# Kernel optimization log

Measured on AMD Instinct MI355X. Metric: run time of the kernel, lower is better.

Reference implementation:

```python
import jax, jax.numpy as jnp
import numpy as np

V, FN, CIN, HID, PTS = 50000, 100000, 3, 256, 10000
TEMP = 0.1
EPS = 1e-20


def line_mesh_graph(f, Vn):
    # f: [F,3] int triangles. Build the 'line mesh': one node per unique mesh edge.
    fe = jnp.concatenate([f[:, :2], f[:, 1:], f[:, jnp.array([2, 0])]], 0)  # [3F,2]
    fe = jnp.sort(fe, axis=1)
    keys = fe[:, 0] * Vn + fe[:, 1]                       # [3F] unique key per undirected edge
    ukeys, inv = jnp.unique(keys, return_inverse=True)
    edge_node = jnp.stack([ukeys // Vn, ukeys % Vn], -1)  # [E,2] endpoints of each edge-node
    E = ukeys.shape[0]
    feid = inv.reshape(3, -1).T                           # [F,3] edge-node id per face edge
    # line-graph connectivity: edges of the same face are mutual neighbors, plus self-loops
    srcs, dsts = [], []
    for i, j in ((0, 1), (1, 0), (1, 2), (2, 1), (2, 0), (0, 2)):
        srcs.append(feid[:, i]); dsts.append(feid[:, j])
    loop = jnp.arange(E)
    edge = jnp.stack([jnp.concatenate(srcs + [loop]), jnp.concatenate(dsts + [loop])], 0)  # [2,NE]
    return edge, edge_node, keys


def gsn_conv(x, edge, Ws, Wn, b):
    # GSNConv stand-in: self transform + mean-aggregated neighbor transform
    s, d = edge[0], edge[1]
    N = x.shape[0]
    deg = jax.ops.segment_sum(jnp.ones_like(s, x.dtype), d, num_segments=N)
    agg = jax.ops.segment_sum(x[s], d, num_segments=N) / jnp.clip(deg, 1.0)[:, None]
    return x @ Ws + agg @ Wn + b


def gumbel_mask(logits, temperature, num, key):
    U = jax.random.uniform(key, logits.shape)
    g = -jnp.log(-jnp.log(U + EPS) + EPS)
    y = jax.nn.softmax((logits + g) / temperature, -1)[:, 0]  # [E]
    _, ind = jax.lax.top_k(y, num)
    y_hard = jnp.zeros_like(y).at[ind].set(1.0)
    mask = jax.lax.stop_gradient(y_hard - y) + y              # straight-through one-hot
    return mask, y_hard == 1.0


def mesh_collapse(f, keys, pool_edge, Vn):
    # Vectorized replacement of the per-pool-edge python loop: hash-join pooled edge keys
    # against all 3F face-edge keys via sorted search.
    PE = pool_edge.shape[0]
    pool_idx = jnp.arange(Vn, Vn + PE)
    edge_keys = keys.reshape(3, -1).T                     # [F,3] (cols: e01,e12,e20)
    pk = pool_edge[:, 0] * Vn + pool_edge[:, 1]
    order = jnp.argsort(pk); pks = pk[order]
    flat = edge_keys.reshape(-1)
    pos = jnp.clip(jnp.searchsorted(pks, flat), 0, PE - 1)
    found = pks[pos] == flat
    pei = jnp.where(found, pool_idx[order[pos]], -1).reshape(-1, 3)  # pool_edge_idx [F,3]
    fm = found.reshape(-1, 3)
    pen = fm.sum(1)                                       # pool_edge_num per face
    psi = (fm * jnp.arange(3)).sum(1)                     # pool_start_idx per face
    vv = jnp.stack([f[:, 0], pei[:, 0], f[:, 1], pei[:, 1], f[:, 2], pei[:, 2]], -1)
    nf0 = f[pen == 0]
    fv1 = vv[pen == 1]; s1 = psi[pen == 1]
    fv1 = jnp.concatenate([fv1[s1 == 0], jnp.roll(fv1[s1 == 1], -2, 1), jnp.roll(fv1[s1 == 2], 2, 1)], 0)
    nf1 = jnp.concatenate([jnp.stack([fv1[:, 0], fv1[:, 1], fv1[:, 4]], -1),
                           jnp.stack([fv1[:, 1], fv1[:, 2], fv1[:, 4]], -1)], 0)
    fv2 = vv[pen == 2]; s2 = psi[pen == 2]
    fv2 = jnp.concatenate([fv2[s2 == 1], jnp.roll(fv2[s2 == 2], 2, 1), jnp.roll(fv2[s2 == 3], -2, 1)], 0)
    nf2 = jnp.concatenate([jnp.stack([fv2[:, 0], fv2[:, 1], fv2[:, 4]], -1),
                           jnp.stack([fv2[:, 1], fv2[:, 2], fv2[:, 3]], -1),
                           jnp.stack([fv2[:, 1], fv2[:, 3], fv2[:, 4]], -1)], 0)
    fv3 = vv[pen == 3]
    nf3 = jnp.concatenate([jnp.stack([fv3[:, 0], fv3[:, 1], fv3[:, 5]], -1),
                           jnp.stack([fv3[:, 1], fv3[:, 2], fv3[:, 3]], -1),
                           jnp.stack([fv3[:, 1], fv3[:, 3], fv3[:, 5]], -1),
                           jnp.stack([fv3[:, 3], fv3[:, 4], fv3[:, 5]], -1)], 0)
    new_faces = jnp.concatenate([nf0, nf1, nf2, nf3], 0)
    ne = jnp.concatenate([new_faces[:, :2], new_faces[:, 1:], new_faces[:, jnp.array([2, 0])]], 0)
    ai = jnp.arange(Vn + PE)
    ne = jnp.concatenate([jnp.stack([ai, ai], -1), ne], 0)
    return new_faces, ne.T


def setup_inputs():
    key = jax.random.key(0)
    ks = jax.random.split(key, 10)
    s1 = 1.0 / np.sqrt(CIN); s2 = 1.0 / np.sqrt(HID)
    return {
        'input': jax.random.normal(ks[0], (1, V, CIN), jnp.float32),
        'face': jax.random.randint(ks[1], (1, FN, 3), 0, V),
        'coord': jax.random.normal(ks[2], (1, V, 3), jnp.float32),
        'detail_points': jax.random.normal(ks[3], (1, PTS, 3), jnp.float32),
        'div': 5,
        'W1s': jax.random.normal(ks[4], (CIN, HID), jnp.float32) * s1,
        'W1n': jax.random.normal(ks[5], (CIN, HID), jnp.float32) * s1,
        'b1': jnp.zeros((HID,), jnp.float32),
        'W2s': jax.random.normal(ks[6], (HID, 2), jnp.float32) * s2,
        'W2n': jax.random.normal(ks[7], (HID, 2), jnp.float32) * s2,
        'b2': jnp.zeros((2,), jnp.float32),
    }


def reference(input, face, coord, detail_points, div, W1s, W1n, b1, W2s, W2n, b2):
    # B=1 (data-dependent per-sample output sizes make batch stacking only valid then)
    x0, f = input[0], face[0]
    Vn = x0.shape[0]
    edge, edge_node, keys = line_mesh_graph(f, Vn)
    xe = 0.5 * (x0[edge_node[:, 0]] + x0[edge_node[:, 1]])   # edge-node features [E,C]
    h = jax.nn.relu(gsn_conv(xe, edge, W1s, W1n, b1))
    out = jax.nn.sigmoid(gsn_conv(h, edge, W2s, W2n, b2))    # [E,2]
    mask, pool_ind = gumbel_mask(out, TEMP, out.shape[0] // div, jax.random.key(42))
    pool_edge = edge_node[pool_ind]                          # [PE,2]
    new_faces, new_edges = mesh_collapse(f, keys, pool_edge, Vn)
    return edge_node[None], new_faces[None], new_edges[None], mask[None]
```

## Files before the change

kernel.cpp:

```cpp
#include <hip/hip_runtime.h>
#include <stdint.h>

typedef uint32_t u32;
typedef uint64_t u64;

#define VN 50000
#define FN 100000
#define K3F 300000
#define EMAX 300000
#define NB1 1172
#define NBC 98
#define NBH 293

#define W_A      0u
#define W_B      300000u
#define W_PA     600000u
#define W_PB     900000u
#define W_FLAGS  1200000u
#define W_RANKU  1500000u
#define W_UKEYS  1800000u
#define W_SEGOFF 2100000u
#define W_FEID   2400004u
#define W_XE     2700004u
#define W_PK     3600004u
#define W_P      3700004u
#define W_Q      4300004u
#define W_Y      4900004u
#define W_YMAP   5200004u
#define W_TFLAG  5500004u
#define W_TIER   5800004u
#define W_SEL    6100004u
#define W_SELR   6400004u
#define W_CAT    6700004u
#define W_CATR   6800004u
#define W_NFI    6900004u
#define W_HIST   8100004u
#define W_SUMS   8400100u
#define W_CATH   8404196u
#define W_SCAL   8405220u

#define S_E 0
#define S_NUM 1
#define S_PFX 2
#define S_KREM 3
#define S_TU 4
#define S_R 5
#define S_NF 6
#define S_NEN 7
#define S_O1 8
#define S_O2 9
#define S_O3 10
#define S_RS 16
#define S_GS 24
#define S_GP 32

__device__ __forceinline__ void tf2x32(u32 x0, u32 x1, u32& o0, u32& o1) {
  const u32 ks0 = 0u, ks1 = 42u, ks2 = 0x1BD11BDAu ^ 0u ^ 42u;
  x0 += ks0; x1 += ks1;
#define TFR(r) { x0 += x1; x1 = (x1<<(r))|(x1>>(32-(r))); x1 ^= x0; }
  TFR(13) TFR(15) TFR(26) TFR(6)   x0 += ks1; x1 += ks2 + 1u;
  TFR(17) TFR(29) TFR(16) TFR(24)  x0 += ks2; x1 += ks0 + 2u;
  TFR(13) TFR(15) TFR(26) TFR(6)   x0 += ks0; x1 += ks1 + 3u;
  TFR(17) TFR(29) TFR(16) TFR(24)  x0 += ks1; x1 += ks2 + 4u;
  TFR(13) TFR(15) TFR(26) TFR(6)   x0 += ks2; x1 += ks0 + 5u;
#undef TFR
  o0 = x0; o1 = x1;
}

__global__ void scan_blocks(const u32* __restrict__ in, u32* __restrict__ out,
                            u32* __restrict__ sums, int n) {
  __shared__ u32 lds[256];
  int t = threadIdx.x;
  int base = blockIdx.x*1024 + t*4;
  u32 v[4]; u32 tot = 0;
  for (int k = 0; k < 4; ++k) { v[k] = (base+k < n) ? in[base+k] : 0u; tot += v[k]; }
  lds[t] = tot; __syncthreads();
  for (int o = 1; o < 256; o <<= 1) {
    u32 x = (t >= o) ? lds[t-o] : 0u; __syncthreads();
    lds[t] += x; __syncthreads();
  }
  u32 excl = lds[t] - tot;
  if (t == 255) sums[blockIdx.x] = lds[255];
  u32 run = excl;
  for (int k = 0; k < 4; ++k) { if (base+k < n) out[base+k] = run; run += v[k]; }
}

__global__ void scan_sums(u32* __restrict__ s, int nb) {
  __shared__ u32 lds[256];
  __shared__ u32 carry;
  int t = threadIdx.x;
  if (t == 0) carry = 0;
  __syncthreads();
  for (int base = 0; base < nb; base += 1024) {
    int idx = base + t*4;
    u32 v[4]; u32 tot = 0;
    for (int k = 0; k < 4; ++k) { v[k] = (idx+k < nb) ? s[idx+k] : 0u; tot += v[k]; }
    lds[t] = tot; __syncthreads();
    for (int o = 1; o < 256; o <<= 1) {
      u32 x = (t >= o) ? lds[t-o] : 0u; __syncthreads();
      lds[t] += x; __syncthreads();
    }
    u32 excl = lds[t] - tot;
    u32 ctot = lds[255];
    u32 c = carry;
    __syncthreads();
    u32 run = c + excl;
    for (int k = 0; k < 4; ++k) { if (idx+k < nb) s[idx+k] = run; run += v[k]; }
    if (t == 0) carry = c + ctot;
    __syncthreads();
  }
}

__global__ void scan_add(u32* __restrict__ out, const u32* __restrict__ sums, int n) {
  int base = blockIdx.x*1024 + threadIdx.x*4;
  u32 a = sums[blockIdx.x];
  for (int k = 0; k < 4; ++k) if (base+k < n) out[base+k] += a;
}

__global__ void k_rhist(const u32* __restrict__ keys, u32* __restrict__ hist,
                        int n, int shift, int nb) {
  __shared__ u32 h[256];
  int t = threadIdx.x;
  h[t] = 0; __syncthreads();
  int i = blockIdx.x*256 + t;
  if (i < n) atomicAdd(&h[(keys[i]>>shift)&255u], 1u);
  __syncthreads();
  hist[(u32)t*nb + blockIdx.x] = h[t];
}

__global__ void k_rscat(const u32* __restrict__ keys, const u32* __restrict__ pay,
                        u32* __restrict__ okeys, u32* __restrict__ opay,
                        const u32* __restrict__ hist, int n, int shift, int nb, int haspay) {
  __shared__ u64 ball[4][8];
  __shared__ u64 vmask[4];
  int t = threadIdx.x, w = t>>6, lane = t&63;
  int i = blockIdx.x*256 + t;
  bool valid = i < n;
  u32 k = valid ? keys[i] : 0u;
  u32 d = (k>>shift)&255u;
  for (int bit = 0; bit < 8; ++bit) {
    u64 bm = __ballot(valid && ((d>>bit)&1u));
    if (lane == 0) ball[w][bit] = bm;
  }
  u64 vb = __ballot(valid ? 1 : 0);
  if (lane == 0) vmask[w] = vb;
  __syncthreads();
  if (valid) {
    u32 rank = 0;
    for (int ww = 0; ww < w; ++ww) {
      u64 m = vmask[ww];
      for (int bit = 0; bit < 8; ++bit) { u64 bb = ball[ww][bit]; m &= ((d>>bit)&1u) ? bb : ~bb; }
      rank += (u32)__popcll(m);
    }
    u64 m = vmask[w];
    for (int bit = 0; bit < 8; ++bit) { u64 bb = ball[w][bit]; m &= ((d>>bit)&1u) ? bb : ~bb; }
    rank += (u32)__popcll(m & ((1ull<<lane)-1ull));
    u32 pos = hist[d*(u32)nb + blockIdx.x] + rank;
    okeys[pos] = k;
    if (haspay) opay[pos] = pay[i];
  }
}

__global__ void k_keys(const int* __restrict__ face, u32* __restrict__ keys,
                       u32* __restrict__ pay) {
  int i = blockIdx.x*256 + threadIdx.x;
  if (i >= K3F) return;
  int s = i / FN, f = i - s*FN;
  int v0 = face[f*3 + s];
  int v1 = face[f*3 + (s == 2 ? 0 : s+1)];
  int a = min(v0, v1), b = max(v0, v1);
  u32 key = (u32)a * (u32)VN + (u32)b;
  keys[i] = key ^ 0x80000000u;
  pay[i] = (u32)i;
}

__global__ void k_uflag(const u32* __restrict__ sk, u32* __restrict__ flags) {
  int i = blockIdx.x*256 + threadIdx.x;
  if (i >= K3F) return;
  flags[i] = (i == 0 || sk[i] != sk[i-1]) ? 1u : 0u;
}

__global__ void k_uwrite(const u32* __restrict__ sk, const u32* __restrict__ flags,
                         const u32* __restrict__ rank, const u32* __restrict__ pay,
                         u32* __restrict__ ukeys, u32* __restrict__ segoff,
                         u32* __restrict__ feid,
                         u32* __restrict__ scal, const int* __restrict__ divp) {
  int p = blockIdx.x*256 + threadIdx.x;
  if (p >= K3F) return;
  u32 fl = flags[p], rk = rank[p];
  if (fl) { ukeys[rk] = sk[p]; segoff[rk] = (u32)p; }
  u32 id = rk - 1u + fl;
  u32 i = pay[p];
  u32 s = i / FN, f = i - s*FN;
  feid[f*3 + s] = id;
  if (p == K3F-1) {
    u32 E = rk + fl;
    scal[S_E] = E; scal[S_NUM] = E / (u32)divp[0];
    segoff[E] = (u32)K3F;
  }
}

__global__ void k_ennode(const u32* __restrict__ ukeys, const u32* __restrict__ scal,
                         const float* __restrict__ x,
                         float* __restrict__ xe, float* __restrict__ dout) {
  int e = blockIdx.x*256 + threadIdx.x;
  if (e >= (int)scal[S_E]) return;
  int k = (int)(ukeys[e] ^ 0x80000000u);
  long long kk = (long long)k;
  long long qq = (kk - (kk < 0 ? (long long)(VN-1) : 0ll)) / VN;
  int q = (int)qq;
  int r = (int)(kk - qq * VN);
  dout[2*e]   = (float)q;
  dout[2*e+1] = (float)r;
  u32 i0 = (u32)(q < 0 ? q + VN : q);
  u32 i1 = (u32)r;
  for (int c = 0; c < 3; ++c) xe[e*3+c] = 0.5f*(x[i0*3+c] + x[i1*3+c]);
}

__global__ void k_pack(const float* __restrict__ W1s, const float* __restrict__ W1n,
                       const float* __restrict__ b1,
                       const float* __restrict__ W2s, const float* __restrict__ W2n,
                       float* __restrict__ pk) {
  int h = threadIdx.x;
  if (h >= 256) return;
  float* p = pk + h*12;
  p[0] = W1s[h]; p[1] = W1s[256+h]; p[2] = W1s[512+h];
  p[3] = W1n[h]; p[4] = W1n[256+h]; p[5] = W1n[512+h];
  p[6] = b1[h];
  p[7] = W2s[2*h]; p[8] = W2s[2*h+1];
  p[9] = W2n[2*h]; p[10] = W2n[2*h+1];
  p[11] = 0.0f;
}

__device__ __forceinline__ void agg_neighbors(int e, u32 st, u32 en,
                                              const u32* __restrict__ pay,
                                              const u32* __restrict__ feid,
                                              const float* __restrict__ v, int stride,
                                              float* acc0, float* acc1, float* acc2) {
  const int sslot[6] = {0,1,1,2,2,0};
  const int dslot[6] = {1,0,2,1,0,2};
  float c0 = 0.f, c1 = 0.f, c2 = 0.f;
  for (int b = 0; b < 6; ++b) {
    int j = dslot[b], isl = sslot[b];
    for (u32 p = st; p < en; ++p) {
      u32 i = pay[p];
      u32 s = i / FN;
      if ((int)s == j) {
        u32 f = i - s*FN;
        u32 u = feid[f*3 + isl];
        c0 += v[u*stride]; c1 += v[u*stride+1]; if (stride == 3) c2 += v[u*stride+2];
      }
    }
  }
  c0 += v[e*stride]; c1 += v[e*stride+1]; if (stride == 3) c2 += v[e*stride+2];
  *acc0 = c0; *acc1 = c1; *acc2 = c2;
}

__global__ void k_l12(const float* __restrict__ xe, const u32* __restrict__ segoff,
                      const u32* __restrict__ pay, const u32* __restrict__ feid,
                      const u32* __restrict__ scal, const float* __restrict__ pk,
                      float* __restrict__ P, float* __restrict__ Q) {
  int e = blockIdx.x*256 + threadIdx.x;
  if (e >= (int)scal[S_E]) return;
  u32 st = segoff[e], en = segoff[e+1];
  float c0, c1, c2;
  agg_neighbors(e, st, en, pay, feid, xe, 3, &c0, &c1, &c2);
  float x0 = xe[e*3], x1 = xe[e*3+1], x2 = xe[e*3+2];
  float dg = (float)(2u*(en - st) + 1u);
  float m0 = c0/dg, m1 = c1/dg, m2 = c2/dg;
  float p0 = 0.f, p1 = 0.f, q0 = 0.f, q1 = 0.f;
#pragma unroll 8
  for (int hh = 0; hh < 256; ++hh) {
    const float* w = pk + hh*12;
    float s1 = x0*w[0] + x1*w[1] + x2*w[2];
    float s2 = m0*w[3] + m1*w[4] + m2*w[5];
    float h = fmaxf(s1 + s2 + w[6], 0.0f);
    p0 += h*w[7];  p1 += h*w[8];
    q0 += h*w[9];  q1 += h*w[10];
  }
  P[2*e] = p0; P[2*e+1] = p1; Q[2*e] = q0; Q[2*e+1] = q1;
}

__global__ void k_scores(const float* __restrict__ P, const float* __restrict__ Q,
                         const u32* __restrict__ segoff, const u32* __restrict__ pay,
                         const u32* __restrict__ feid,
                         const float* __restrict__ b2, const u32* __restrict__ scal,
                         float* __restrict__ Y, u32* __restrict__ ymap) {
  int e = blockIdx.x*256 + threadIdx.x;
  u32 E = scal[S_E];
  if (e >= (int)E) return;
  u32 st = segoff[e], en = segoff[e+1];
  float a0, a1, dummy;
  agg_neighbors(e, st, en, pay, feid, Q, 2, &a0, &a1, &dummy);
  float dg = (float)(2u*(en - st) + 1u);
  float z0 = P[2*e]   + a0/dg + b2[0];
  float z1 = P[2*e+1] + a1/dg + b2[1];
  float l0 = 1.0f/(1.0f + expf(-z0));
  float l1 = 1.0f/(1.0f + expf(-z1));
  u32 g0b, g1b;
  { u32 o0,o1; tf2x32(0u, 2u*(u32)e,      o0, o1); g0b = o0 ^ o1; }
  { u32 o0,o1; tf2x32(0u, 2u*(u32)e + 1u, o0, o1); g1b = o0 ^ o1; }
  float U0 = __uint_as_float((g0b>>9) | 0x3f800000u) - 1.0f;
  float U1 = __uint_as_float((g1b>>9) | 0x3f800000u) - 1.0f;
  float g0 = -logf(-logf(U0 + 1e-20f) + 1e-20f);
  float g1 = -logf(-logf(U1 + 1e-20f) + 1e-20f);
  float A0 = (l0 + g0)/0.1f;
  float A1 = (l1 + g1)/0.1f;
  float mx = fmaxf(A0, A1);
  float e0 = expf(A0-mx), e1 = expf(A1-mx);
  float y = e0/(e0+e1);
  Y[e] = y;
  ymap[e] = __float_as_uint(y) | 0x80000000u;
}

__global__ void k_tkinit(u32* __restrict__ scal, u32* __restrict__ hist) {
  int t = threadIdx.x;
  if (t < 256) hist[t] = 0u;
  if (t == 0) { scal[S_PFX] = 0u; scal[S_KREM] = scal[S_NUM]; }
}

__global__ void k_tkhist(const u32* __restrict__ ymap, const u32* __restrict__ scal,
                         u32* __restrict__ hist, int byte) {
  __shared__ u32 h[256];
  int t = threadIdx.x;
  h[t] = 0u; __syncthreads();
  int E = (int)scal[S_E];
  u32 pfx = scal[S_PFX];
  int base = blockIdx.x*1024;
  for (int k = 0; k < 4; ++k) {
    int e = base + k*256 + t;
    if (e < E) {
      u32 u = ymap[e];
      bool match = (byte == 3) || ((u >> ((byte+1)*8)) == pfx);
      if (match) atomicAdd(&h[(u >> (byte*8)) & 255u], 1u);
    }
  }
  __syncthreads();
  u32 c = h[t];
  if (c) atomicAdd(&hist[t], c);
}

__global__ void k_tksel(u32* __restrict__ scal, u32* __restrict__ hist, int byte) {
  if (threadIdx.x != 0 || blockIdx.x != 0) return;
  u32 krem = scal[S_KREM], pfx = scal[S_PFX];
  u32 chosen = 0;
  for (int b = 255; b >= 0; --b) {
    u32 c = hist[b];
    if (krem <= c) { chosen = (u32)b; break; }
    krem -= c;
  }
  pfx = (pfx << 8) | chosen;
  scal[S_PFX] = pfx; scal[S_KREM] = krem;
  if (byte == 0) { scal[S_TU] = pfx; scal[S_R] = krem; }
  for (int i = 0; i < 256; ++i) hist[i] = 0u;
}

__global__ void k_tflag(const u32* __restrict__ ymap, const u32* __restrict__ scal,
                        u32* __restrict__ tf) {
  int e = blockIdx.x*256 + threadIdx.x;
  if (e >= EMAX) return;
  tf[e] = (e < (int)scal[S_E] && ymap[e] == scal[S_TU]) ? 1u : 0u;
}

__global__ void k_sel(const u32* __restrict__ ymap, const u32* __restrict__ tier,
                      const u32* __restrict__ scal, u32* __restrict__ sel) {
  int e = blockIdx.x*256 + threadIdx.x;
  if (e >= EMAX) return;
  u32 v = 0;
  if (e < (int)scal[S_E]) {
    u32 u = ymap[e];
    v = (u > scal[S_TU]) || (u == scal[S_TU] && tier[e] < scal[S_R]);
  }
  sel[e] = v ? 1u : 0u;
}

__global__ void k_cat(const u32* __restrict__ feid, const u32* __restrict__ sel,
                      u32* __restrict__ cat) {
  int f = blockIdx.x*256 + threadIdx.x;
  if (f >= FN) return;
  u32 m0 = sel[feid[f*3]], m1 = sel[feid[f*3+1]], m2 = sel[feid[f*3+2]];
  u32 pen = m0 + m1 + m2;
  u32 psi = m1 + 2u*m2;
  u32 c = (pen == 0) ? 0u : (pen == 1) ? (1u+psi) : (pen == 2) ? (3u+psi) : 7u;
  cat[f] = c;
}

__global__ void k_cathist(const u32* __restrict__ cat, u32* __restrict__ ch) {
  __shared__ u32 h[8];
  int t = threadIdx.x;
  if (t < 8) h[t] = 0u;
  __syncthreads();
  int base = blockIdx.x*1024 + t*4;
  for (int k = 0; k < 4; ++k) if (base+k < FN) atomicAdd(&h[cat[base+k]], 1u);
  __syncthreads();
  if (t < 8) ch[(u32)t*NBC + blockIdx.x] = h[t];
}

__global__ void k_catoff(u32* __restrict__ ch, u32* __restrict__ scal) {
  if (threadIdx.x || blockIdx.x) return;
  u32 tot[8];
  for (int c = 0; c < 8; ++c) { u32 s = 0; for (int b = 0; b < NBC; ++b) s += ch[c*NBC+b]; tot[c] = s; }
  u32 run = 0;
  for (int i = 0; i < 8*NBC; ++i) { u32 v = ch[i]; ch[i] = run; run += v; }
  u32 n0 = tot[0], n1 = tot[1]+tot[2]+tot[3], n2 = tot[4]+tot[5]+tot[6], n3 = tot[7];
  u32 NF = n0 + 2u*n1 + 3u*n2 + 4u*n3;
  u32 E = scal[S_E], num = scal[S_NUM];
  u32 NEn = (u32)VN + num + 3u*NF;
  scal[S_NF] = NF; scal[S_NEN] = NEn;
  scal[S_O1] = 2u*E;
  scal[S_O2] = 2u*E + 3u*NF;
  scal[S_O3] = 2u*E + 3u*NF + 2u*NEn;
  u32 RS[8] = {0u, n0,n0,n0, n0+2u*n1, n0+2u*n1, n0+2u*n1, n0+2u*n1+3u*n2};
  u32 GS[8] = {0u, n1,n1,n1, n2,n2,n2, n3};
  u32 GP[8] = {0u, n0,n0,n0, n0+n1, n0+n1, n0+n1, n0+n1+n2};
  for (int i = 0; i < 8; ++i) { scal[S_RS+i] = RS[i]; scal[S_GS+i] = GS[i]; scal[S_GP+i] = GP[i]; }
}

__global__ void k_catrank(const u32* __restrict__ cat, const u32* __restrict__ ch,
                          u32* __restrict__ cr) {
  __shared__ u32 lds[256];
  int t = threadIdx.x;
  int base = blockIdx.x*1024 + t*4;
  u32 cc[4], loc[4];
  u32 cnt[8] = {0,0,0,0,0,0,0,0};
  for (int k = 0; k < 4; ++k) {
    int i = base + k;
    if (i < FN) { u32 c = cat[i]; cc[k] = c; loc[k] = cnt[c]++; }
    else cc[k] = 8u;
  }
  u32 tb[8];
  for (int c = 0; c < 8; ++c) {
    lds[t] = cnt[c]; __syncthreads();
    for (int o = 1; o < 256; o <<= 1) {
      u32 x = (t >= o) ? lds[t-o] : 0u; __syncthreads();
      lds[t] += x; __syncthreads();
    }
    tb[c] = lds[t] - cnt[c];
    __syncthreads();
  }
  for (int k = 0; k < 4; ++k) {
    int i = base + k;
    if (i < FN) { u32 c = cc[k]; cr[i] = ch[c*NBC + blockIdx.x] + tb[c] + loc[k]; }
  }
}

__global__ void k_wfaces(const int* __restrict__ face, const u32* __restrict__ cat,
                         const u32* __restrict__ cr, const u32* __restrict__ feid,
                         const u32* __restrict__ selr, const u32* __restrict__ scal,
                         int* __restrict__ nfi, float* __restrict__ dout) {
  int f = blockIdx.x*256 + threadIdx.x;
  if (f >= FN) return;
  const int nfc[8] = {1,2,2,2,3,3,3,4};
  const int tri[8][4][3] = {
    {{0,2,4},{0,0,0},{0,0,0},{0,0,0}},
    {{0,1,4},{1,2,4},{0,0,0},{0,0,0}},
    {{2,3,0},{3,4,0},{0,0,0},{0,0,0}},
    {{4,5,2},{5,0,2},{0,0,0},{0,0,0}},
    {{0,1,4},{1,2,3},{1,3,4},{0,0,0}},
    {{4,5,2},{5,0,1},{5,1,2},{0,0,0}},
    {{2,3,0},{3,4,5},{3,5,0},{0,0,0}},
    {{0,1,5},{1,2,3},{1,3,5},{3,4,5}}};
  u32 c = cat[f];
  int cv[6];
  cv[0] = face[f*3];   cv[2] = face[f*3+1]; cv[4] = face[f*3+2];
  cv[1] = VN + (int)selr[feid[f*3]];
  cv[3] = VN + (int)selr[feid[f*3+1]];
  cv[5] = VN + (int)selr[feid[f*3+2]];
  u32 g  = cr[f] - scal[S_GP + c];
  u32 o1 = scal[S_O1];
  for (int j = 0; j < nfc[c]; ++j) {
    u32 row = scal[S_RS + c] + (u32)j*scal[S_GS + c] + g;
    for (int m = 0; m < 3; ++m) {
      int v = cv[tri[c][j][m]];
      nfi[row*3 + m] = v;
      dout[o1 + row*3 + m] = (float)v;
    }
  }
}

__global__ void k_wne(const int* __restrict__ nfi, const u32* __restrict__ scal,
                      float* __restrict__ dout) {
  int i = blockIdx.x*256 + threadIdx.x;
  u32 NEn = scal[S_NEN];
  if (i >= (int)NEn) return;
  u32 NF = scal[S_NF];
  u32 Vp = (u32)VN + scal[S_NUM];
  u32 o2 = scal[S_O2];
  int a, b;
  if ((u32)i < Vp) { a = i; b = i; }
  else {
    u32 j = (u32)i - Vp;
    u32 blk = j / NF, r = j - blk*NF;
    int i0 = (blk == 0) ? 0 : (blk == 1) ? 1 : 2;
    int i1 = (blk == 0) ? 1 : (blk == 1) ? 2 : 0;
    a = nfi[r*3 + i0]; b = nfi[r*3 + i1];
  }
  dout[o2 + i] = (float)a;
  dout[o2 + NEn + i] = (float)b;
}

__global__ void k_wmask(const u32* __restrict__ sel, const float* __restrict__ Y,
                        const u32* __restrict__ scal, float* __restrict__ dout) {
  int e = blockIdx.x*256 + threadIdx.x;
  if (e >= (int)scal[S_E]) return;
  float y = Y[e];
  float yh = sel[e] ? 1.0f : 0.0f;
  dout[scal[S_O3] + e] = (yh - y) + y;
}

static void run_scan(u32* in, u32* out, u32* sums, int n, hipStream_t st) {
  int nb = (n + 1023) / 1024;
  scan_blocks<<<nb, 256, 0, st>>>(in, out, sums, n);
  scan_sums<<<1, 256, 0, st>>>(sums, nb);
  scan_add<<<nb, 256, 0, st>>>(out, sums, n);
}

static void radix_pass(u32* kin, u32* pin, u32* kout, u32* pout, u32* hist, u32* sums,
                       int n, int nb, int shift, bool haspay, hipStream_t st) {
  k_rhist<<<nb, 256, 0, st>>>(kin, hist, n, shift, nb);
  run_scan(hist, hist, sums, nb*256, st);
  k_rscat<<<nb, 256, 0, st>>>(kin, pin, kout, pout, hist, n, shift, nb, haspay ? 1 : 0);
}

extern "C" void kernel_launch(void* const* d_in, const int* in_sizes, int n_in,
                              void* d_out, int out_size, void* d_ws, size_t ws_size,
                              hipStream_t stream) {
  const float* x    = (const float*)d_in[0];
  const int*   face = (const int*)d_in[1];
  const int*   divp = (const int*)d_in[4];
  const float* W1s  = (const float*)d_in[5];
  const float* W1n  = (const float*)d_in[6];
  const float* b1   = (const float*)d_in[7];
  const float* W2s  = (const float*)d_in[8];
  const float* W2n  = (const float*)d_in[9];
  const float* b2   = (const float*)d_in[10];
  float* out = (float*)d_out;
  u32* W = (u32*)d_ws;

  u32 *A = W+W_A, *B = W+W_B, *PA = W+W_PA, *PB = W+W_PB;
  u32 *FL = W+W_FLAGS, *RK = W+W_RANKU, *UK = W+W_UKEYS;
  u32 *HIST = W+W_HIST, *SUMS = W+W_SUMS, *SCAL = W+W_SCAL;

  k_pack<<<1, 256, 0, stream>>>(W1s, W1n, b1, W2s, W2n, (float*)(W+W_PK));

  k_keys<<<NB1, 256, 0, stream>>>(face, A, PA);
  radix_pass(A, PA, B, PB, HIST, SUMS, K3F, NB1,  0, true, stream);
  radix_pass(B, PB, A, PA, HIST, SUMS, K3F, NB1,  8, true, stream);
  radix_pass(A, PA, B, PB, HIST, SUMS, K3F, NB1, 16, true, stream);
  radix_pass(B, PB, A, PA, HIST, SUMS, K3F, NB1, 24, true, stream);
  k_uflag<<<NB1, 256, 0, stream>>>(A, FL);
  run_scan(FL, RK, SUMS, K3F, stream);
  k_uwrite<<<NB1, 256, 0, stream>>>(A, FL, RK, PA, UK, W+W_SEGOFF, W+W_FEID, SCAL, divp);

  k_ennode<<<NB1, 256, 0, stream>>>(UK, SCAL, x, (float*)(W+W_XE), out);

  k_l12<<<NB1, 256, 0, stream>>>((float*)(W+W_XE), W+W_SEGOFF, PA, W+W_FEID, SCAL,
                                 (float*)(W+W_PK), (float*)(W+W_P), (float*)(W+W_Q));
  k_scores<<<NB1, 256, 0, stream>>>((float*)(W+W_P), (float*)(W+W_Q), W+W_SEGOFF, PA,
                                    W+W_FEID, b2, SCAL, (float*)(W+W_Y), W+W_YMAP);

  k_tkinit<<<1, 256, 0, stream>>>(SCAL, HIST);
  for (int byte = 3; byte >= 0; --byte) {
    k_tkhist<<<NBH, 256, 0, stream>>>(W+W_YMAP, SCAL, HIST, byte);
    k_tksel<<<1, 1, 0, stream>>>(SCAL, HIST, byte);
  }
  k_tflag<<<NB1, 256, 0, stream>>>(W+W_YMAP, SCAL, W+W_TFLAG);
  run_scan(W+W_TFLAG, W+W_TIER, SUMS, EMAX, stream);
  k_sel<<<NB1, 256, 0, stream>>>(W+W_YMAP, W+W_TIER, SCAL, W+W_SEL);
  run_scan(W+W_SEL, W+W_SELR, SUMS, EMAX, stream);

  k_cat<<<391, 256, 0, stream>>>(W+W_FEID, W+W_SEL, W+W_CAT);
  k_cathist<<<NBC, 256, 0, stream>>>(W+W_CAT, W+W_CATH);
  k_catoff<<<1, 1, 0, stream>>>(W+W_CATH, SCAL);
  k_catrank<<<NBC, 256, 0, stream>>>(W+W_CAT, W+W_CATH, W+W_CATR);
  k_wfaces<<<391, 256, 0, stream>>>(face, W+W_CAT, W+W_CATR, W+W_FEID, W+W_SELR, SCAL,
                                    (int*)(W+W_NFI), out);
  k_wne<<<5118, 256, 0, stream>>>((int*)(W+W_NFI), SCAL, out);
  k_wmask<<<NB1, 256, 0, stream>>>(W+W_SEL, (float*)(W+W_Y), SCAL, out);
}
```

Before: 381.9 us.

## Fuse scan add-back into consumers and parallelize serial selection kernels

Drops the separate scan_add pass by having consumers (radix scatter, unique write, selection) add the block carry themselves. Unique flags are now computed inside the scan instead of in a separate kernel. The tie-flag scan and the selection-rank scan are merged into one 64-bit packed scan, with the greater-than count in the low half and the tie count in the high half. The single-thread k_tksel and k_catoff kernels become 256-thread LDS scans. Together this cuts launches and global passes, at the cost of extra loads in consumers and 64-bit LDS traffic.

```diff
diff --git a/kernel.cpp b/kernel.cpp
--- a/kernel.cpp
+++ b/kernel.cpp
@@ -11,33 +11,32 @@
 #define NB1 1172
 #define NBC 98
 #define NBH 293
+#define NBS 293
 
 #define W_A      0u
 #define W_B      300000u
 #define W_PA     600000u
 #define W_PB     900000u
-#define W_FLAGS  1200000u
-#define W_RANKU  1500000u
-#define W_UKEYS  1800000u
-#define W_SEGOFF 2100000u
-#define W_FEID   2400004u
-#define W_XE     2700004u
-#define W_PK     3600004u
-#define W_P      3700004u
-#define W_Q      4300004u
-#define W_Y      4900004u
-#define W_YMAP   5200004u
-#define W_TFLAG  5500004u
-#define W_TIER   5800004u
-#define W_SEL    6100004u
-#define W_SELR   6400004u
-#define W_CAT    6700004u
-#define W_CATR   6800004u
-#define W_NFI    6900004u
-#define W_HIST   8100004u
-#define W_SUMS   8400100u
-#define W_CATH   8404196u
-#define W_SCAL   8405220u
+#define W_RANKU  1200000u
+#define W_UKEYS  1500000u
+#define W_SEGOFF 1800000u
+#define W_FEID   2100004u
+#define W_XE     2400004u
+#define W_PK     3300004u
+#define W_P      3400004u
+#define W_Q      4000004u
+#define W_Y      4600004u
+#define W_YMAP   4900004u
+#define W_T64    5200004u
+#define W_SEL    5800068u
+#define W_SELR   6100068u
+#define W_CAT    6400068u
+#define W_CATR   6500068u
+#define W_NFI    6600068u
+#define W_HIST   7800068u
+#define W_SUMS   8100100u
+#define W_CATH   8104196u
+#define W_SCAL   8105220u
 
 #define S_E 0
 #define S_NUM 1
@@ -74,6 +73,29 @@
   int base = blockIdx.x*1024 + t*4;
   u32 v[4]; u32 tot = 0;
   for (int k = 0; k < 4; ++k) { v[k] = (base+k < n) ? in[base+k] : 0u; tot += v[k]; }
+  lds[t] = tot; __syncthreads();
+  for (int o = 1; o < 256; o <<= 1) {
+    u32 x = (t >= o) ? lds[t-o] : 0u; __syncthreads();
+    lds[t] += x; __syncthreads();
+  }
+  u32 excl = lds[t] - tot;
+  if (t == 255) sums[blockIdx.x] = lds[255];
+  u32 run = excl;
+  for (int k = 0; k < 4; ++k) { if (base+k < n) out[base+k] = run; run += v[k]; }
+}
+
+__global__ void scan_flagblocks(const u32* __restrict__ sk, u32* __restrict__ out,
+                                u32* __restrict__ sums, int n) {
+  __shared__ u32 lds[256];
+  int t = threadIdx.x;
+  int base = blockIdx.x*1024 + t*4;
+  u32 v[4]; u32 tot = 0;
+  for (int k = 0; k < 4; ++k) {
+    int i = base + k;
+    u32 f = 0;
+    if (i < n) f = (i == 0 || sk[i-1] != sk[i]) ? 1u : 0u;
+    v[k] = f; tot += f;
+  }
   lds[t] = tot; __syncthreads();
   for (int o = 1; o < 256; o <<= 1) {
     u32 x = (t >= o) ? lds[t-o] : 0u; __syncthreads();
@@ -111,10 +133,67 @@
   }
 }
 
-__global__ void scan_add(u32* __restrict__ out, const u32* __restrict__ sums, int n) {
-  int base = blockIdx.x*1024 + threadIdx.x*4;
-  u32 a = sums[blockIdx.x];
-  for (int k = 0; k < 4; ++k) if (base+k < n) out[base+k] += a;
+__global__ void scan64_src(const u32* __restrict__ ymap, const u32* __restrict__ scal,
+                           u64* __restrict__ part, u64* __restrict__ sums) {
+  __shared__ u64 lds[256];
+  int t = threadIdx.x;
+  int base = blockIdx.x*1024 + t*4;
+  int E = (int)scal[S_E];
+  u32 TU = scal[S_TU];
+  u64 v[4]; u64 tot = 0;
+  for (int k = 0; k < 4; ++k) {
+    int e = base + k;
+    u64 val = 0;
+    if (e < E) {
+      u32 u = ymap[e];
+      if (u > TU) val = 1ull;
+      else if (u == TU) val = 1ull << 32;
+    }
+    v[k] = val; tot += val;
+  }
+  lds[t] = tot; __syncthreads();
+  for (int o = 1; o < 256; o <<= 1) {
+    u64 x = (t >= o) ? lds[t-o] : 0ull; __syncthreads();
+    lds[t] += x; __syncthreads();
+  }
+  u64 excl = lds[t] - tot;
+  if (t == 255) sums[blockIdx.x] = lds[255];
+  u64 run = excl;
+  for (int k = 0; k < 4; ++k) { part[base+k] = run; run += v[k]; }
+}
+
+__global__ void scan64_sums(u64* __restrict__ s, int nb) {
+  __shared__ u64 lds[256];
+  int t = threadIdx.x;
+  int idx = t*4;
+  u64 v[4]; u64 tot = 0;
+  for (int k = 0; k < 4; ++k) { v[k] = (idx+k < nb) ? s[idx+k] : 0ull; tot += v[k]; }
+  lds[t] = tot; __syncthreads();
+  for (int o = 1; o < 256; o <<= 1) {
+    u64 x = (t >= o) ? lds[t-o] : 0ull; __syncthreads();
+    lds[t] += x; __syncthreads();
+  }
+  u64 excl = lds[t] - tot;
+  u64 run = excl;
+  for (int k = 0; k < 4; ++k) { if (idx+k < nb) s[idx+k] = run; run += v[k]; }
+}
+
+__global__ void k_sel2(const u32* __restrict__ ymap, const u64* __restrict__ part,
+                       const u64* __restrict__ sums, const u32* __restrict__ scal,
+                       u32* __restrict__ sel, u32* __restrict__ selr) {
+  int e = blockIdx.x*256 + threadIdx.x;
+  if (e >= EMAX) return;
+  int E = (int)scal[S_E];
+  u32 TU = scal[S_TU], R = scal[S_R];
+  u64 pre = part[e] + sums[e>>10];
+  u32 GTpre = (u32)pre, TIEpre = (u32)(pre >> 32);
+  u32 v = 0;
+  if (e < E) {
+    u32 u = ymap[e];
+    v = (u > TU) || (u == TU && TIEpre < R);
+  }
+  sel[e] = v ? 1u : 0u;
+  selr[e] = GTpre + min(TIEpre, R);
 }
 
 __global__ void k_rhist(const u32* __restrict__ keys, u32* __restrict__ hist,
@@ -130,7 +209,8 @@
 
 __global__ void k_rscat(const u32* __restrict__ keys, const u32* __restrict__ pay,
                         u32* __restrict__ okeys, u32* __restrict__ opay,
-                        const u32* __restrict__ hist, int n, int shift, int nb, int haspay) {
+                        const u32* __restrict__ hist, const u32* __restrict__ sums,
+                        int n, int shift, int nb) {
   __shared__ u64 ball[4][8];
   __shared__ u64 vmask[4];
   int t = threadIdx.x, w = t>>6, lane = t&63;
@@ -155,9 +235,10 @@
     u64 m = vmask[w];
     for (int bit = 0; bit < 8; ++bit) { u64 bb = ball[w][bit]; m &= ((d>>bit)&1u) ? bb : ~bb; }
     rank += (u32)__popcll(m & ((1ull<<lane)-1ull));
-    u32 pos = hist[d*(u32)nb + blockIdx.x] + rank;
+    u32 h = d*(u32)nb + blockIdx.x;
+    u32 pos = hist[h] + sums[h>>10] + rank;
     okeys[pos] = k;
-    if (haspay) opay[pos] = pay[i];
+    opay[pos] = pay[i];
   }
 }
 
@@ -174,21 +255,17 @@
   pay[i] = (u32)i;
 }
 
-__global__ void k_uflag(const u32* __restrict__ sk, u32* __restrict__ flags) {
-  int i = blockIdx.x*256 + threadIdx.x;
-  if (i >= K3F) return;
-  flags[i] = (i == 0 || sk[i] != sk[i-1]) ? 1u : 0u;
-}
-
-__global__ void k_uwrite(const u32* __restrict__ sk, const u32* __restrict__ flags,
-                         const u32* __restrict__ rank, const u32* __restrict__ pay,
+__global__ void k_uwrite(const u32* __restrict__ sk, const u32* __restrict__ rankp,
+                         const u32* __restrict__ sums, const u32* __restrict__ pay,
                          u32* __restrict__ ukeys, u32* __restrict__ segoff,
                          u32* __restrict__ feid,
                          u32* __restrict__ scal, const int* __restrict__ divp) {
   int p = blockIdx.x*256 + threadIdx.x;
   if (p >= K3F) return;
-  u32 fl = flags[p], rk = rank[p];
-  if (fl) { ukeys[rk] = sk[p]; segoff[rk] = (u32)p; }
+  u32 cur = sk[p];
+  u32 fl = (p == 0 || sk[p-1] != cur) ? 1u : 0u;
+  u32 rk = rankp[p] + sums[p>>10];
+  if (fl) { ukeys[rk] = cur; segoff[rk] = (u32)p; }
   u32 id = rk - 1u + fl;
   u32 i = pay[p];
   u32 s = i / FN, f = i - s*FN;
@@ -341,37 +418,29 @@
 }
 
 __global__ void k_tksel(u32* __restrict__ scal, u32* __restrict__ hist, int byte) {
-  if (threadIdx.x != 0 || blockIdx.x != 0) return;
-  u32 krem = scal[S_KREM], pfx = scal[S_PFX];
-  u32 chosen = 0;
-  for (int b = 255; b >= 0; --b) {
-    u32 c = hist[b];
-    if (krem <= c) { chosen = (u32)b; break; }
-    krem -= c;
-  }
-  pfx = (pfx << 8) | chosen;
-  scal[S_PFX] = pfx; scal[S_KREM] = krem;
-  if (byte == 0) { scal[S_TU] = pfx; scal[S_R] = krem; }
-  for (int i = 0; i < 256; ++i) hist[i] = 0u;
-}
-
-__global__ void k_tflag(const u32* __restrict__ ymap, const u32* __restrict__ scal,
-                        u32* __restrict__ tf) {
-  int e = blockIdx.x*256 + threadIdx.x;
-  if (e >= EMAX) return;
-  tf[e] = (e < (int)scal[S_E] && ymap[e] == scal[S_TU]) ? 1u : 0u;
-}
-
-__global__ void k_sel(const u32* __restrict__ ymap, const u32* __restrict__ tier,
-                      const u32* __restrict__ scal, u32* __restrict__ sel) {
-  int e = blockIdx.x*256 + threadIdx.x;
-  if (e >= EMAX) return;
-  u32 v = 0;
-  if (e < (int)scal[S_E]) {
-    u32 u = ymap[e];
-    v = (u > scal[S_TU]) || (u == scal[S_TU] && tier[e] < scal[S_R]);
-  }
-  sel[e] = v ? 1u : 0u;
+  __shared__ u32 s2[256];
+  __shared__ u32 chosen_s;
+  int t = threadIdx.x;
+  u32 v = hist[t];
+  hist[t] = 0u;
+  s2[t] = v;
+  if (t == 0) chosen_s = 0u;
+  __syncthreads();
+  for (int o = 1; o < 256; o <<= 1) {
+    u32 x = (t + o < 256) ? s2[t+o] : 0u; __syncthreads();
+    s2[t] += x; __syncthreads();
+  }
+  u32 krem = scal[S_KREM];
+  if (s2[t] >= krem) atomicMax(&chosen_s, (u32)t);
+  __syncthreads();
+  if (t == 0) {
+    u32 chosen = chosen_s;
+    u32 sufnext = (chosen < 255u) ? s2[chosen+1] : 0u;
+    u32 newkrem = krem - sufnext;
+    u32 pfx = (scal[S_PFX] << 8) | chosen;
+    scal[S_PFX] = pfx; scal[S_KREM] = newkrem;
+    if (byte == 0) { scal[S_TU] = pfx; scal[S_R] = newkrem; }
+  }
 }
 
 __global__ void k_cat(const u32* __restrict__ feid, const u32* __restrict__ sel,
@@ -397,23 +466,48 @@
 }
 
 __global__ void k_catoff(u32* __restrict__ ch, u32* __restrict__ scal) {
-  if (threadIdx.x || blockIdx.x) return;
-  u32 tot[8];
-  for (int c = 0; c < 8; ++c) { u32 s = 0; for (int b = 0; b < NBC; ++b) s += ch[c*NBC+b]; tot[c] = s; }
-  u32 run = 0;
-  for (int i = 0; i < 8*NBC; ++i) { u32 v = ch[i]; ch[i] = run; run += v; }
-  u32 n0 = tot[0], n1 = tot[1]+tot[2]+tot[3], n2 = tot[4]+tot[5]+tot[6], n3 = tot[7];
-  u32 NF = n0 + 2u*n1 + 3u*n2 + 4u*n3;
-  u32 E = scal[S_E], num = scal[S_NUM];
-  u32 NEn = (u32)VN + num + 3u*NF;
-  scal[S_NF] = NF; scal[S_NEN] = NEn;
-  scal[S_O1] = 2u*E;
-  scal[S_O2] = 2u*E + 3u*NF;
-  scal[S_O3] = 2u*E + 3u*NF + 2u*NEn;
-  u32 RS[8] = {0u, n0,n0,n0, n0+2u*n1, n0+2u*n1, n0+2u*n1, n0+2u*n1+3u*n2};
-  u32 GS[8] = {0u, n1,n1,n1, n2,n2,n2, n3};
-  u32 GP[8] = {0u, n0,n0,n0, n0+n1, n0+n1, n0+n1, n0+n1+n2};
-  for (int i = 0; i < 8; ++i) { scal[S_RS+i] = RS[i]; scal[S_GS+i] = GS[i]; scal[S_GP+i] = GP[i]; }
+  __shared__ u32 lds[256];
+  __shared__ u32 ex[1024];
+  int t = threadIdx.x;
+  u32 v[4]; u32 tot = 0;
+  for (int k = 0; k < 4; ++k) {
+    int i = t*4 + k;
+    u32 x = (i < 8*NBC) ? ch[i] : 0u;
+    v[k] = x; tot += x;
+  }
+  lds[t] = tot; __syncthreads();
+  for (int o = 1; o < 256; o <<= 1) {
+    u32 x = (t >= o) ? lds[t-o] : 0u; __syncthreads();
+    lds[t] += x; __syncthreads();
+  }
+  u32 excl = lds[t] - tot;
+  u32 run = excl;
+  for (int k = 0; k < 4; ++k) { ex[t*4+k] = run; run += v[k]; }
+  __syncthreads();
+  for (int k = 0; k < 4; ++k) {
+    int i = t*4 + k;
+    if (i < 8*NBC) ch[i] = ex[i];
+  }
+  if (t == 0) {
+    u32 total = lds[255];
+    u32 bnd[9];
+    for (int c = 0; c < 8; ++c) bnd[c] = ex[c*NBC];
+    bnd[8] = total;
+    u32 tot8[8];
+    for (int c = 0; c < 8; ++c) tot8[c] = bnd[c+1] - bnd[c];
+    u32 n0 = tot8[0], n1 = tot8[1]+tot8[2]+tot8[3], n2 = tot8[4]+tot8[5]+tot8[6], n3 = tot8[7];
+    u32 NF = n0 + 2u*n1 + 3u*n2 + 4u*n3;
+    u32 E = scal[S_E], num = scal[S_NUM];
+    u32 NEn = (u32)VN + num + 3u*NF;
+    scal[S_NF] = NF; scal[S_NEN] = NEn;
+    scal[S_O1] = 2u*E;
+    scal[S_O2] = 2u*E + 3u*NF;
+    scal[S_O3] = 2u*E + 3u*NF + 2u*NEn;
+    u32 RS[8] = {0u, n0,n0,n0, n0+2u*n1, n0+2u*n1, n0+2u*n1, n0+2u*n1+3u*n2};
+    u32 GS[8] = {0u, n1,n1,n1, n2,n2,n2, n3};
+    u32 GP[8] = {0u, n0,n0,n0, n0+n1, n0+n1, n0+n1, n0+n1+n2};
+    for (int i = 0; i < 8; ++i) { scal[S_RS+i] = RS[i]; scal[S_GS+i] = GS[i]; scal[S_GP+i] = GP[i]; }
+  }
 }
 
 __global__ void k_catrank(const u32* __restrict__ cat, const u32* __restrict__ ch,
@@ -508,18 +602,14 @@
   dout[scal[S_O3] + e] = (yh - y) + y;
 }
 
-static void run_scan(u32* in, u32* out, u32* sums, int n, hipStream_t st) {
-  int nb = (n + 1023) / 1024;
-  scan_blocks<<<nb, 256, 0, st>>>(in, out, sums, n);
-  scan_sums<<<1, 256, 0, st>>>(sums, nb);
-  scan_add<<<nb, 256, 0, st>>>(out, sums, n);
-}
-
 static void radix_pass(u32* kin, u32* pin, u32* kout, u32* pout, u32* hist, u32* sums,
-                       int n, int nb, int shift, bool haspay, hipStream_t st) {
+                       int n, int nb, int shift, hipStream_t st) {
   k_rhist<<<nb, 256, 0, st>>>(kin, hist, n, shift, nb);
-  run_scan(hist, hist, sums, nb*256, st);
-  k_rscat<<<nb, 256, 0, st>>>(kin, pin, kout, pout, hist, n, shift, nb, haspay ? 1 : 0);
+  int nscan = nb*256;
+  int nbs = (nscan + 1023)/1024;
+  scan_blocks<<<nbs, 256, 0, st>>>(hist, hist, sums, nscan);
+  scan_sums<<<1, 256, 0, st>>>(sums, nbs);
+  k_rscat<<<nb, 256, 0, st>>>(kin, pin, kout, pout, hist, sums, n, shift, nb);
 }
 
 extern "C" void kernel_launch(void* const* d_in, const int* in_sizes, int n_in,
@@ -538,19 +628,21 @@
   u32* W = (u32*)d_ws;
 
   u32 *A = W+W_A, *B = W+W_B, *PA = W+W_PA, *PB = W+W_PB;
-  u32 *FL = W+W_FLAGS, *RK = W+W_RANKU, *UK = W+W_UKEYS;
+  u32 *RK = W+W_RANKU, *UK = W+W_UKEYS;
   u32 *HIST = W+W_HIST, *SUMS = W+W_SUMS, *SCAL = W+W_SCAL;
+  u64 *T64 = (u64*)(W+W_T64);
+  u64 *SUMS64 = (u64*)(W+W_SUMS);
 
   k_pack<<<1, 256, 0, stream>>>(W1s, W1n, b1, W2s, W2n, (float*)(W+W_PK));
 
   k_keys<<<NB1, 256, 0, stream>>>(face, A, PA);
-  radix_pass(A, PA, B, PB, HIST, SUMS, K3F, NB1,  0, true, stream);
-  radix_pass(B, PB, A, PA, HIST, SUMS, K3F, NB1,  8, true, stream);
-  radix_pass(A, PA, B, PB, HIST, SUMS, K3F, NB1, 16, true, stream);
-  radix_pass(B, PB, A, PA, HIST, SUMS, K3F, NB1, 24, true, stream);
-  k_uflag<<<NB1, 256, 0, stream>>>(A, FL);
-  run_scan(FL, RK, SUMS, K3F, stream);
-  k_uwrite<<<NB1, 256, 0, stream>>>(A, FL, RK, PA, UK, W+W_SEGOFF, W+W_FEID, SCAL, divp);
+  radix_pass(A, PA, B, PB, HIST, SUMS, K3F, NB1,  0, stream);
+  radix_pass(B, PB, A, PA, HIST, SUMS, K3F, NB1,  8, stream);
+  radix_pass(A, PA, B, PB, HIST, SUMS, K3F, NB1, 16, stream);
+  radix_pass(B, PB, A, PA, HIST, SUMS, K3F, NB1, 24, stream);
+  scan_flagblocks<<<NBS, 256, 0, stream>>>(A, RK, SUMS, K3F);
+  scan_sums<<<1, 256, 0, stream>>>(SUMS, NBS);
+  k_uwrite<<<NB1, 256, 0, stream>>>(A, RK, SUMS, PA, UK, W+W_SEGOFF, W+W_FEID, SCAL, divp);
 
   k_ennode<<<NB1, 256, 0, stream>>>(UK, SCAL, x, (float*)(W+W_XE), out);
 
@@ -562,16 +654,15 @@
   k_tkinit<<<1, 256, 0, stream>>>(SCAL, HIST);
   for (int byte = 3; byte >= 0; --byte) {
     k_tkhist<<<NBH, 256, 0, stream>>>(W+W_YMAP, SCAL, HIST, byte);
-    k_tksel<<<1, 1, 0, stream>>>(SCAL, HIST, byte);
-  }
-  k_tflag<<<NB1, 256, 0, stream>>>(W+W_YMAP, SCAL, W+W_TFLAG);
-  run_scan(W+W_TFLAG, W+W_TIER, SUMS, EMAX, stream);
-  k_sel<<<NB1, 256, 0, stream>>>(W+W_YMAP, W+W_TIER, SCAL, W+W_SEL);
-  run_scan(W+W_SEL, W+W_SELR, SUMS, EMAX, stream);
+    k_tksel<<<1, 256, 0, stream>>>(SCAL, HIST, byte);
+  }
+  scan64_src<<<NBS, 256, 0, stream>>>(W+W_YMAP, SCAL, T64, SUMS64);
+  scan64_sums<<<1, 256, 0, stream>>>(SUMS64, NBS);
+  k_sel2<<<NB1, 256, 0, stream>>>(W+W_YMAP, T64, SUMS64, SCAL, W+W_SEL, W+W_SELR);
 
   k_cat<<<391, 256, 0, stream>>>(W+W_FEID, W+W_SEL, W+W_CAT);
   k_cathist<<<NBC, 256, 0, stream>>>(W+W_CAT, W+W_CATH);
-  k_catoff<<<1, 1, 0, stream>>>(W+W_CATH, SCAL);
+  k_catoff<<<1, 256, 0, stream>>>(W+W_CATH, SCAL);
   k_catrank<<<NBC, 256, 0, stream>>>(W+W_CAT, W+W_CATH, W+W_CATR);
   k_wfaces<<<391, 256, 0, stream>>>(face, W+W_CAT, W+W_CATR, W+W_FEID, W+W_SELR, SCAL,
                                     (int*)(W+W_NFI), out);
```

Result: faster. 329.2 us (-13.8%).
